# Optimization experiments

Hardware: AMD Instinct MI355X
Metric: run time of the kernel (lower is better)

Reference implementation:

```python
import jax, jax.numpy as jnp
import numpy as np

EPSILON = 0.1
GAMMA = 1.0
RHO = 0.5
STOPERR = 1e-6
NUMITERMAX = 100
FI = GAMMA / (GAMMA + EPSILON)  # exponent for semi-relaxed KL side


def setup_inputs() -> dict:
    key = jax.random.key(0)
    logits = jax.random.normal(key, (16, 4096, 1024), dtype=jnp.float32)
    return {"logits": logits}


def reference(logits):
    B, n, k = logits.shape
    K = k + 1  # extra 'dustbin' column with zero cost
    cost = -jax.nn.log_softmax(logits, axis=-1)                       # [B,n,k]
    expand_cost = jnp.concatenate([cost, jnp.zeros((B, n, 1), cost.dtype)], axis=-1)
    Q = jnp.exp(-expand_cost / EPSILON)                               # [B,n,K]
    Qt = Q.transpose(0, 2, 1)                                         # [B,K,n]
    Pa = jnp.full((B, n, 1), 1.0 / n, Q.dtype)
    Pb = jnp.full((B, K, 1), RHO / k, Q.dtype).at[:, -1, :].set(1.0 - RHO)
    a0 = jnp.zeros((B, n, 1), Q.dtype)
    b0 = jnp.full((B, K, 1), 1.0 / K, Q.dtype)

    def cond(state):
        _, _, err, it = state
        return jnp.logical_and(err > STOPERR, it < NUMITERMAX)

    def body(state):
        _, b, _, it = state
        a = Pa / jnp.matmul(Q, b)                                     # [B,n,1]
        b_new = Pb / jnp.matmul(Qt, a)                                # [B,K,1]
        b_new = b_new.at[:, :-1, :].set(jnp.power(b_new[:, :-1, :], FI))
        err = jnp.sqrt(jnp.sum((b_new - b) ** 2))
        return (a, b_new, err, it + 1)

    a, b, err, it = jax.lax.while_loop(
        cond, body, (a0, b0, jnp.asarray(1.0, Q.dtype), jnp.asarray(0)))

    plan = a * Q * b.transpose(0, 2, 1) * n                           # [B,n,K]
    return plan[:, :, :-1].astype(jnp.float32)                        # drop dustbin col
```

## Files before the change

kernel.cpp:

```cpp
#include <hip/hip_runtime.h>
#include <math.h>


namespace {
constexpr int   Bn      = 16;
constexpr int   Kc      = 1024;
constexpr int   KK      = 1025;
constexpr int   BSTR    = 1028;
constexpr int   ROWS    = 65536;
constexpr int   NBLK    = 512;
constexpr int   TPB     = 512;
constexpr int   SUBS    = 32;
constexpr int   RPB     = 128;
constexpr float PA      = 1.0f / 4096.0f;
constexpr float PB_LOW  = (float)(0.5 / 1024.0);
constexpr float PB_DUST = 0.5f;
constexpr float FI_F    = (float)(1.0 / 1.1);
constexpr float STOP    = 1e-6f;
constexpr int   NITER   = 100;
constexpr float LOG2E   = 1.44269504088896340736f;
constexpr float ILOG2E  = 0.69314718055994530942f;
constexpr float TLOG2E  = 14.4269504088896340736f;
constexpr float B0      = (float)(1.0 / 1025.0);
}

typedef __attribute__((ext_vector_type(8))) unsigned short ushort8;

__device__ __forceinline__ float wredsum(float v) {
#pragma unroll
  for (int m = 32; m >= 1; m >>= 1) v += __shfl_xor(v, m, 64);
  return v;
}
__device__ __forceinline__ float wredmax(float v) {
#pragma unroll
  for (int m = 32; m >= 1; m >>= 1) v = fmaxf(v, __shfl_xor(v, m, 64));
  return v;
}
__device__ __forceinline__ unsigned short f2bf(float x) {
  unsigned int u = __float_as_uint(x);
  return (unsigned short)((u + 0x7FFFu + ((u >> 16) & 1u)) >> 16);
}
__device__ __forceinline__ float bf2f(unsigned short h) {
  return __uint_as_float(((unsigned int)h) << 16);
}

__global__ void k_init(float* __restrict__ bstore, float* __restrict__ e2vec) {
  int tid = blockIdx.x * blockDim.x + threadIdx.x;
  int stride = gridDim.x * blockDim.x;
  for (int i = tid; i < Bn * BSTR; i += stride) {
    int j = i % BSTR;
    bstore[i] = (j < KK) ? B0 : 0.0f;
  }
  for (int i = tid; i < NITER * Bn; i += stride)
    e2vec[i] = (i == 0) ? 1.0f : 0.0f;
}

template <int MODE>
__global__ __launch_bounds__(512, 4) void k_step(
    const float* __restrict__ x, unsigned short* __restrict__ Qb,
    float* __restrict__ lsev, float* __restrict__ avec,
    float* __restrict__ bstore,
    const float* __restrict__ partIn, float* __restrict__ partOut,
    const float* __restrict__ sumaIn, float* __restrict__ sumaOut,
    float* __restrict__ e2vec, float* __restrict__ out, const int t) {
  __shared__ float bls[1026];
  __shared__ float cpart[8][1024];
  __shared__ float sred[8];
  __shared__ int sstop;
  const int tid = threadIdx.x, wave = tid >> 6, lane = tid & 63;
  const int blk = blockIdx.x, b = blk >> 5, sub = blk & 31;
  const int j2 = tid << 1;

  if constexpr (MODE != 0) {
    if (tid == 0) {
      float s = 0.0f;
#pragma unroll
      for (int j = 0; j < Bn; ++j) s += e2vec[(t - 1) * Bn + j];
      sstop = (!(sqrtf(s) > STOP)) ? 1 : 0;
    }
    __syncthreads();
    if constexpr (MODE == 1) { if (sstop) return; }

    if (MODE == 2 && sstop) {
      bls[j2]     = bstore[b * BSTR + j2];
      bls[j2 + 1] = bstore[b * BSTR + j2 + 1];
      if (tid == 0) bls[1024] = bstore[b * BSTR + 1024];
    } else {
      const float* pb = partIn + ((size_t)b << 15);
      float s0 = 0.0f, s1 = 0.0f;
#pragma unroll 8
      for (int sb = 0; sb < SUBS; ++sb) {
        const float2 v = *(const float2*)(pb + (sb << 10) + j2);
        s0 += v.x; s1 += v.y;
      }
      const float bn0 = exp2f(FI_F * log2f(PB_LOW / s0));
      const float bn1 = exp2f(FI_F * log2f(PB_LOW / s1));
      bls[j2] = bn0; bls[j2 + 1] = bn1;
      if (wave == 0) {
        float sa = (lane < SUBS) ? sumaIn[(b << 5) + lane] : 0.0f;
        sa = wredsum(sa);
        if (lane == 0) bls[1024] = PB_DUST / sa;
      }
      if constexpr (MODE == 1) {
        if (sub == 0) {
          const float bo0 = bstore[b * BSTR + j2];
          const float bo1 = bstore[b * BSTR + j2 + 1];
          float e2 = (bn0 - bo0) * (bn0 - bo0) + (bn1 - bo1) * (bn1 - bo1);
          const float ew = wredsum(e2);
          if (lane == 0) sred[wave] = ew;
          __syncthreads();
          if (tid == 0) {
            float tt = 0.0f;
#pragma unroll
            for (int w = 0; w < 8; ++w) tt += sred[w];
            const float bd = bls[1024], bod = bstore[b * BSTR + 1024];
            tt += (bd - bod) * (bd - bod);
            e2vec[t * Bn + b] = tt;
            bstore[b * BSTR + 1024] = bd;
          }
          bstore[b * BSTR + j2]     = bn0;
          bstore[b * BSTR + j2 + 1] = bn1;
        }
      }
    }
    __syncthreads();
  }

  if constexpr (MODE == 2) {
    float4 bb[4];
#pragma unroll
    for (int s = 0; s < 4; ++s) bb[s] = *(const float4*)&bls[(lane << 4) + (s << 2)];
    const int rowBase = blk * RPB + wave * 16;
    for (int r = 0; r < 16; ++r) {
      const int row = rowBase + r;
      const float lse = lsev[row];
      const float sc = avec[row] * 4096.0f;
      const float4* xp = (const float4*)(x + ((size_t)row << 10));
      float4* op = (float4*)(out + ((size_t)row << 10));
#pragma unroll
      for (int s = 0; s < 4; ++s) {
        const float4 v = xp[(lane << 2) + s];
        float4 o;
        o.x = exp2f((v.x - lse) * TLOG2E) * sc * bb[s].x;
        o.y = exp2f((v.y - lse) * TLOG2E) * sc * bb[s].y;
        o.z = exp2f((v.z - lse) * TLOG2E) * sc * bb[s].z;
        o.w = exp2f((v.w - lse) * TLOG2E) * sc * bb[s].w;
        op[(lane << 2) + s] = o;
      }
    }
    return;
  }

  float4 bb[4];
  float bdust;
  if constexpr (MODE == 0) {
    const float4 c = make_float4(B0, B0, B0, B0);
#pragma unroll
    for (int s = 0; s < 4; ++s) bb[s] = c;
    bdust = B0;
  } else {
#pragma unroll
    for (int s = 0; s < 4; ++s) bb[s] = *(const float4*)&bls[(lane << 4) + (s << 2)];
    bdust = bls[1024];
  }

  float acc[16];
#pragma unroll
  for (int e = 0; e < 16; ++e) acc[e] = 0.0f;
  float sal = 0.0f;

  const int rowBase = blk * RPB + wave * 16;
#pragma unroll 4
  for (int r = 0; r < 16; ++r) {
    float q[16];
    if constexpr (MODE == 0) {
      const float4* xp = (const float4*)(x + ((size_t)(rowBase + r) << 10));
      float4 v[4];
#pragma unroll
      for (int s = 0; s < 4; ++s) v[s] = xp[(lane << 2) + s];
      float m = -1e30f;
#pragma unroll
      for (int s = 0; s < 4; ++s)
        m = fmaxf(m, fmaxf(fmaxf(v[s].x, v[s].y), fmaxf(v[s].z, v[s].w)));
      m = wredmax(m);
      float su = 0.0f;
#pragma unroll
      for (int s = 0; s < 4; ++s)
        su += exp2f((v[s].x - m) * LOG2E) + exp2f((v[s].y - m) * LOG2E) +
              exp2f((v[s].z - m) * LOG2E) + exp2f((v[s].w - m) * LOG2E);
      su = wredsum(su);
      const float lse = m + log2f(su) * ILOG2E;
      if (lane == 0) lsev[rowBase + r] = lse;
      ushort8 qa, qb2;
#pragma unroll
      for (int s = 0; s < 4; ++s) {
        const unsigned short u0 = f2bf(exp2f((v[s].x - lse) * TLOG2E));
        const unsigned short u1 = f2bf(exp2f((v[s].y - lse) * TLOG2E));
        const unsigned short u2 = f2bf(exp2f((v[s].z - lse) * TLOG2E));
        const unsigned short u3 = f2bf(exp2f((v[s].w - lse) * TLOG2E));
        if (s < 2) { qa[s*4+0]=u0; qa[s*4+1]=u1; qa[s*4+2]=u2; qa[s*4+3]=u3; }
        else { qb2[(s-2)*4+0]=u0; qb2[(s-2)*4+1]=u1; qb2[(s-2)*4+2]=u2; qb2[(s-2)*4+3]=u3; }
        q[s*4+0]=bf2f(u0); q[s*4+1]=bf2f(u1); q[s*4+2]=bf2f(u2); q[s*4+3]=bf2f(u3);
      }
      ushort8* qp = (ushort8*)(Qb + ((size_t)(rowBase + r) << 10));
      qp[lane * 2] = qa; qp[lane * 2 + 1] = qb2;
    } else {
      const ushort8* qp = (const ushort8*)(Qb + ((size_t)(rowBase + r) << 10));
      const ushort8 qa = qp[lane * 2], qb2 = qp[lane * 2 + 1];
#pragma unroll
      for (int e = 0; e < 8; ++e) { q[e] = bf2f(qa[e]); q[8 + e] = bf2f(qb2[e]); }
    }

    float p = 0.0f;
#pragma unroll
    for (int s = 0; s < 4; ++s)
      p += q[s * 4 + 0] * bb[s].x + q[s * 4 + 1] * bb[s].y +
           q[s * 4 + 2] * bb[s].z + q[s * 4 + 3] * bb[s].w;

    const float inner = wredsum(p) + bdust;
    const float a = PA / inner;
    if (lane == 0) { avec[rowBase + r] = a; sal += a; }
#pragma unroll
    for (int e = 0; e < 16; ++e) acc[e] += q[e] * a;
  }
  if (lane == 0) sred[wave] = sal;

  float4* cp = (float4*)&cpart[wave][lane << 4];
#pragma unroll
  for (int s = 0; s < 4; ++s)
    cp[s] = make_float4(acc[s * 4 + 0], acc[s * 4 + 1], acc[s * 4 + 2], acc[s * 4 + 3]);
  __syncthreads();

  float o0 = 0.0f, o1 = 0.0f;
#pragma unroll
  for (int w = 0; w < 8; ++w) { o0 += cpart[w][j2]; o1 += cpart[w][j2 + 1]; }
  *(float2*)(partOut + ((size_t)b << 15) + (sub << 10) + j2) = make_float2(o0, o1);
  if (tid == 0) {
    float ss = 0.0f;
#pragma unroll
    for (int w = 0; w < 8; ++w) ss += sred[w];
    sumaOut[(b << 5) + sub] = ss;
  }
}

extern "C" void kernel_launch(void* const* d_in, const int* in_sizes, int n_in,
                              void* d_out, int out_size, void* d_ws, size_t ws_size,
                              hipStream_t stream) {
  const float* logits = (const float*)d_in[0];
  unsigned short* Qb = (unsigned short*)d_out;
  float* ws = (float*)d_ws;
  float* bstore = ws;
  float* avec   = bstore + Bn * BSTR;
  float* lsev   = avec + ROWS;
  float* partA  = lsev + ROWS;
  float* partB  = partA + (size_t)Bn * SUBS * Kc;
  float* sumaA  = partB + (size_t)Bn * SUBS * Kc;
  float* sumaB  = sumaA + NBLK;
  float* e2vec  = sumaB + NBLK;

  k_init<<<16, 256, 0, stream>>>(bstore, e2vec);
  k_step<0><<<NBLK, TPB, 0, stream>>>(logits, Qb, lsev, avec, bstore,
                                      partA, partA, sumaA, sumaA, e2vec, nullptr, 0);
  for (int t = 1; t < NITER; ++t) {
    const bool odd = (t & 1) != 0;
    k_step<1><<<NBLK, TPB, 0, stream>>>(logits, Qb, lsev, avec, bstore,
                                        odd ? partA : partB, odd ? partB : partA,
                                        odd ? sumaA : sumaB, odd ? sumaB : sumaA,
                                        e2vec, nullptr, t);
  }
  k_step<2><<<NBLK, TPB, 0, stream>>>(logits, Qb, lsev, avec, bstore,
                                      partB, partA, sumaB, sumaA, e2vec,
                                      (float*)d_out, NITER);
}
```

Baseline: 3.245 ms.

## Prefetch Q rows before the b-reduction, drop the max-subtraction, add a bf16-Q final pass

In the iteration kernel, eight Q rows per wave are loaded into registers before the partial-sum reduction and barrier, and the rest are software-pipelined, so global load latency overlaps the b update. The first pass drops the row max from the log-sum-exp and uses the known uniform b0 to compute a directly as a sum of q. When the workspace is large enough, Q is stored there and the final pass rebuilds the plan from bf16 Q instead of re-reading the logits and recomputing exp. The stop-flag check now runs in parallel with the b computation instead of behind its own barrier. Risks: overflow of exp without the max for large logits, higher register pressure, and a bf16-rounded output.

```diff
diff --git a/kernel.cpp b/kernel.cpp
--- a/kernel.cpp
+++ b/kernel.cpp
@@ -22,6 +22,9 @@
 constexpr float ILOG2E  = 0.69314718055994530942f;
 constexpr float TLOG2E  = 14.4269504088896340736f;
 constexpr float B0      = (float)(1.0 / 1025.0);
+constexpr size_t QBYTES = (size_t)ROWS * 1024 * 2;
+constexpr size_t FWORDS = (size_t)Bn * BSTR + 2 * ROWS +
+                          2 * (size_t)Bn * SUBS * Kc + 2 * NBLK + NITER * Bn;
 }
 
 typedef __attribute__((ext_vector_type(8))) unsigned short ushort8;
@@ -29,11 +32,6 @@
 __device__ __forceinline__ float wredsum(float v) {
 #pragma unroll
   for (int m = 32; m >= 1; m >>= 1) v += __shfl_xor(v, m, 64);
-  return v;
-}
-__device__ __forceinline__ float wredmax(float v) {
-#pragma unroll
-  for (int m = 32; m >= 1; m >>= 1) v = fmaxf(v, __shfl_xor(v, m, 64));
   return v;
 }
 __device__ __forceinline__ unsigned short f2bf(float x) {
@@ -42,6 +40,25 @@
 }
 __device__ __forceinline__ float bf2f(unsigned short h) {
   return __uint_as_float(((unsigned int)h) << 16);
+}
+
+__device__ __forceinline__ void consume_row(
+    const ushort8 qa, const ushort8 qb2, const float4* bb, const float bdust,
+    float* acc, float& sal, float* __restrict__ avec, const int row,
+    const int lane) {
+  float q[16];
+#pragma unroll
+  for (int e = 0; e < 8; ++e) { q[e] = bf2f(qa[e]); q[8 + e] = bf2f(qb2[e]); }
+  float p = 0.0f;
+#pragma unroll
+  for (int s = 0; s < 4; ++s)
+    p += q[s * 4 + 0] * bb[s].x + q[s * 4 + 1] * bb[s].y +
+         q[s * 4 + 2] * bb[s].z + q[s * 4 + 3] * bb[s].w;
+  const float inner = wredsum(p) + bdust;
+  const float a = PA / inner;
+  if (lane == 0) { avec[row] = a; sal += a; }
+#pragma unroll
+  for (int e = 0; e < 16; ++e) acc[e] += q[e] * a;
 }
 
 __global__ void k_init(float* __restrict__ bstore, float* __restrict__ e2vec) {
@@ -66,26 +83,30 @@
   __shared__ float bls[1026];
   __shared__ float cpart[8][1024];
   __shared__ float sred[8];
-  __shared__ int sstop;
+  __shared__ int sstop_s;
   const int tid = threadIdx.x, wave = tid >> 6, lane = tid & 63;
   const int blk = blockIdx.x, b = blk >> 5, sub = blk & 31;
   const int j2 = tid << 1;
-
+  const int rowBase = blk * RPB + wave * 16;
+
+  const ushort8* qrow = (const ushort8*)Qb + ((size_t)rowBase << 7) + (lane << 1);
+  ushort8 qa0, qb0, qa1, qb1, qa2, qb2, qa3, qb3,
+          qa4, qb4, qa5, qb5, qa6, qb6, qa7, qb7;
+#define QLOAD(i, r) do { qa##i = qrow[(r) << 7]; qb##i = qrow[((r) << 7) + 1]; } while (0)
+
+  if constexpr (MODE == 1) {
+    QLOAD(0, 0); QLOAD(1, 1); QLOAD(2, 2); QLOAD(3, 3);
+    QLOAD(4, 4); QLOAD(5, 5); QLOAD(6, 6); QLOAD(7, 7);
+  }
+
+  float bn0 = 0.0f, bn1 = 0.0f;
   if constexpr (MODE != 0) {
-    if (tid == 0) {
-      float s = 0.0f;
-#pragma unroll
-      for (int j = 0; j < Bn; ++j) s += e2vec[(t - 1) * Bn + j];
-      sstop = (!(sqrtf(s) > STOP)) ? 1 : 0;
-    }
-    __syncthreads();
-    if constexpr (MODE == 1) { if (sstop) return; }
-
-    if (MODE == 2 && sstop) {
-      bls[j2]     = bstore[b * BSTR + j2];
-      bls[j2 + 1] = bstore[b * BSTR + j2 + 1];
-      if (tid == 0) bls[1024] = bstore[b * BSTR + 1024];
-    } else {
+    if (wave == 0) {
+      float g = (lane < Bn) ? e2vec[(t - 1) * Bn + lane] : 0.0f;
+      g = wredsum(g);
+      if (lane == 0) sstop_s = (!(sqrtf(g) > STOP)) ? 1 : 0;
+    }
+    {
       const float* pb = partIn + ((size_t)b << 15);
       float s0 = 0.0f, s1 = 0.0f;
 #pragma unroll 8
@@ -93,44 +114,64 @@
         const float2 v = *(const float2*)(pb + (sb << 10) + j2);
         s0 += v.x; s1 += v.y;
       }
-      const float bn0 = exp2f(FI_F * log2f(PB_LOW / s0));
-      const float bn1 = exp2f(FI_F * log2f(PB_LOW / s1));
+      bn0 = exp2f(FI_F * log2f(PB_LOW / s0));
+      bn1 = exp2f(FI_F * log2f(PB_LOW / s1));
       bls[j2] = bn0; bls[j2 + 1] = bn1;
-      if (wave == 0) {
-        float sa = (lane < SUBS) ? sumaIn[(b << 5) + lane] : 0.0f;
-        sa = wredsum(sa);
-        if (lane == 0) bls[1024] = PB_DUST / sa;
-      }
-      if constexpr (MODE == 1) {
-        if (sub == 0) {
-          const float bo0 = bstore[b * BSTR + j2];
-          const float bo1 = bstore[b * BSTR + j2 + 1];
-          float e2 = (bn0 - bo0) * (bn0 - bo0) + (bn1 - bo1) * (bn1 - bo1);
-          const float ew = wredsum(e2);
-          if (lane == 0) sred[wave] = ew;
-          __syncthreads();
-          if (tid == 0) {
-            float tt = 0.0f;
-#pragma unroll
-            for (int w = 0; w < 8; ++w) tt += sred[w];
-            const float bd = bls[1024], bod = bstore[b * BSTR + 1024];
-            tt += (bd - bod) * (bd - bod);
-            e2vec[t * Bn + b] = tt;
-            bstore[b * BSTR + 1024] = bd;
-          }
-          bstore[b * BSTR + j2]     = bn0;
-          bstore[b * BSTR + j2 + 1] = bn1;
+    }
+    if (wave == 1) {
+      float sa = (lane < SUBS) ? sumaIn[(b << 5) + lane] : 0.0f;
+      sa = wredsum(sa);
+      if (lane == 0) bls[1024] = PB_DUST / sa;
+    }
+    __syncthreads();
+    const int sstop = sstop_s;
+    if constexpr (MODE == 1) {
+      if (sstop) return;
+      if (sub == 0) {
+        const float bo0 = bstore[b * BSTR + j2];
+        const float bo1 = bstore[b * BSTR + j2 + 1];
+        float e2 = (bn0 - bo0) * (bn0 - bo0) + (bn1 - bo1) * (bn1 - bo1);
+        const float ew = wredsum(e2);
+        if (lane == 0) sred[wave] = ew;
+        __syncthreads();
+        if (tid == 0) {
+          float tt = 0.0f;
+#pragma unroll
+          for (int w = 0; w < 8; ++w) tt += sred[w];
+          const float bd = bls[1024], bod = bstore[b * BSTR + 1024];
+          tt += (bd - bod) * (bd - bod);
+          e2vec[t * Bn + b] = tt;
+          bstore[b * BSTR + 1024] = bd;
         }
-      }
-    }
-    __syncthreads();
+        __syncthreads();
+        bstore[b * BSTR + j2]     = bn0;
+        bstore[b * BSTR + j2 + 1] = bn1;
+      }
+    } else {
+      if (sstop) {
+        bls[j2]     = bstore[b * BSTR + j2];
+        bls[j2 + 1] = bstore[b * BSTR + j2 + 1];
+        if (tid == 0) bls[1024] = bstore[b * BSTR + 1024];
+      }
+      __syncthreads();
+    }
+  }
+
+  float4 bb[4];
+  float bdust;
+  if constexpr (MODE == 0) {
+    const float4 c = make_float4(B0, B0, B0, B0);
+#pragma unroll
+    for (int s = 0; s < 4; ++s) bb[s] = c;
+    bdust = B0;
+  } else {
+#pragma unroll
+    for (int s = 0; s < 4; ++s) bb[s] = *(const float4*)&bls[(lane << 4) + (s << 2)];
+    bdust = bls[1024];
   }
 
   if constexpr (MODE == 2) {
-    float4 bb[4];
-#pragma unroll
-    for (int s = 0; s < 4; ++s) bb[s] = *(const float4*)&bls[(lane << 4) + (s << 2)];
-    const int rowBase = blk * RPB + wave * 16;
+#pragma unroll 2
     for (int r = 0; r < 16; ++r) {
       const int row = rowBase + r;
       const float lse = lsev[row];
@@ -151,17 +192,27 @@
     return;
   }
 
-  float4 bb[4];
-  float bdust;
-  if constexpr (MODE == 0) {
-    const float4 c = make_float4(B0, B0, B0, B0);
-#pragma unroll
-    for (int s = 0; s < 4; ++s) bb[s] = c;
-    bdust = B0;
-  } else {
-#pragma unroll
-    for (int s = 0; s < 4; ++s) bb[s] = *(const float4*)&bls[(lane << 4) + (s << 2)];
-    bdust = bls[1024];
+  if constexpr (MODE == 3) {
+#pragma unroll 2
+    for (int r = 0; r < 16; ++r) {
+      const int row = rowBase + r;
+      const ushort8 ua = qrow[r << 7], ub = qrow[(r << 7) + 1];
+      const float sc = avec[row] * 4096.0f;
+      float4* op = (float4*)(out + ((size_t)row << 10));
+      float q[16];
+#pragma unroll
+      for (int e = 0; e < 8; ++e) { q[e] = bf2f(ua[e]); q[8 + e] = bf2f(ub[e]); }
+#pragma unroll
+      for (int s = 0; s < 4; ++s) {
+        float4 o;
+        o.x = q[s * 4 + 0] * sc * bb[s].x;
+        o.y = q[s * 4 + 1] * sc * bb[s].y;
+        o.z = q[s * 4 + 2] * sc * bb[s].z;
+        o.w = q[s * 4 + 3] * sc * bb[s].w;
+        op[(lane << 2) + s] = o;
+      }
+    }
+    return;
   }
 
   float acc[16];
@@ -169,62 +220,64 @@
   for (int e = 0; e < 16; ++e) acc[e] = 0.0f;
   float sal = 0.0f;
 
-  const int rowBase = blk * RPB + wave * 16;
-#pragma unroll 4
-  for (int r = 0; r < 16; ++r) {
-    float q[16];
-    if constexpr (MODE == 0) {
-      const float4* xp = (const float4*)(x + ((size_t)(rowBase + r) << 10));
+  if constexpr (MODE == 0) {
+#pragma unroll 2
+    for (int r = 0; r < 16; ++r) {
+      const int row = rowBase + r;
+      const float4* xp = (const float4*)(x + ((size_t)row << 10));
       float4 v[4];
 #pragma unroll
       for (int s = 0; s < 4; ++s) v[s] = xp[(lane << 2) + s];
-      float m = -1e30f;
+      float su = 0.0f;
 #pragma unroll
       for (int s = 0; s < 4; ++s)
-        m = fmaxf(m, fmaxf(fmaxf(v[s].x, v[s].y), fmaxf(v[s].z, v[s].w)));
-      m = wredmax(m);
-      float su = 0.0f;
-#pragma unroll
-      for (int s = 0; s < 4; ++s)
-        su += exp2f((v[s].x - m) * LOG2E) + exp2f((v[s].y - m) * LOG2E) +
-              exp2f((v[s].z - m) * LOG2E) + exp2f((v[s].w - m) * LOG2E);
+        su += exp2f(v[s].x * LOG2E) + exp2f(v[s].y * LOG2E) +
+              exp2f(v[s].z * LOG2E) + exp2f(v[s].w * LOG2E);
       su = wredsum(su);
-      const float lse = m + log2f(su) * ILOG2E;
-      if (lane == 0) lsev[rowBase + r] = lse;
-      ushort8 qa, qb2;
+      const float lse = log2f(su) * ILOG2E;
+      if (lane == 0) lsev[row] = lse;
+      float q[16];
+      ushort8 ua, ub;
 #pragma unroll
       for (int s = 0; s < 4; ++s) {
         const unsigned short u0 = f2bf(exp2f((v[s].x - lse) * TLOG2E));
         const unsigned short u1 = f2bf(exp2f((v[s].y - lse) * TLOG2E));
         const unsigned short u2 = f2bf(exp2f((v[s].z - lse) * TLOG2E));
         const unsigned short u3 = f2bf(exp2f((v[s].w - lse) * TLOG2E));
-        if (s < 2) { qa[s*4+0]=u0; qa[s*4+1]=u1; qa[s*4+2]=u2; qa[s*4+3]=u3; }
-        else { qb2[(s-2)*4+0]=u0; qb2[(s-2)*4+1]=u1; qb2[(s-2)*4+2]=u2; qb2[(s-2)*4+3]=u3; }
+        if (s < 2) { ua[s*4+0]=u0; ua[s*4+1]=u1; ua[s*4+2]=u2; ua[s*4+3]=u3; }
+        else { ub[(s-2)*4+0]=u0; ub[(s-2)*4+1]=u1; ub[(s-2)*4+2]=u2; ub[(s-2)*4+3]=u3; }
         q[s*4+0]=bf2f(u0); q[s*4+1]=bf2f(u1); q[s*4+2]=bf2f(u2); q[s*4+3]=bf2f(u3);
       }
-      ushort8* qp = (ushort8*)(Qb + ((size_t)(rowBase + r) << 10));
-      qp[lane * 2] = qa; qp[lane * 2 + 1] = qb2;
-    } else {
-      const ushort8* qp = (const ushort8*)(Qb + ((size_t)(rowBase + r) << 10));
-      const ushort8 qa = qp[lane * 2], qb2 = qp[lane * 2 + 1];
-#pragma unroll
-      for (int e = 0; e < 8; ++e) { q[e] = bf2f(qa[e]); q[8 + e] = bf2f(qb2[e]); }
-    }
-
-    float p = 0.0f;
-#pragma unroll
-    for (int s = 0; s < 4; ++s)
-      p += q[s * 4 + 0] * bb[s].x + q[s * 4 + 1] * bb[s].y +
-           q[s * 4 + 2] * bb[s].z + q[s * 4 + 3] * bb[s].w;
-
-    const float inner = wredsum(p) + bdust;
-    const float a = PA / inner;
-    if (lane == 0) { avec[rowBase + r] = a; sal += a; }
-#pragma unroll
-    for (int e = 0; e < 16; ++e) acc[e] += q[e] * a;
-  }
+      ushort8* qp = (ushort8*)(Qb + ((size_t)row << 10));
+      qp[lane * 2] = ua; qp[lane * 2 + 1] = ub;
+      float sq = 0.0f;
+#pragma unroll
+      for (int e = 0; e < 16; ++e) sq += q[e];
+      const float inner = (wredsum(sq) + 1.0f) * B0;
+      const float a = PA / inner;
+      if (lane == 0) { avec[row] = a; sal += a; }
+#pragma unroll
+      for (int e = 0; e < 16; ++e) acc[e] += q[e] * a;
+    }
+  } else {
+#define STEP(i, r) do { \
+    consume_row(qa##i, qb##i, bb, bdust, acc, sal, avec, rowBase + (r), lane); \
+  } while (0)
+    STEP(0, 0); QLOAD(0, 8);
+    STEP(1, 1); QLOAD(1, 9);
+    STEP(2, 2); QLOAD(2, 10);
+    STEP(3, 3); QLOAD(3, 11);
+    STEP(4, 4); QLOAD(4, 12);
+    STEP(5, 5); QLOAD(5, 13);
+    STEP(6, 6); QLOAD(6, 14);
+    STEP(7, 7); QLOAD(7, 15);
+    STEP(0, 8);  STEP(1, 9);  STEP(2, 10); STEP(3, 11);
+    STEP(4, 12); STEP(5, 13); STEP(6, 14); STEP(7, 15);
+#undef STEP
+  }
+#undef QLOAD
+
   if (lane == 0) sred[wave] = sal;
-
   float4* cp = (float4*)&cpart[wave][lane << 4];
 #pragma unroll
   for (int s = 0; s < 4; ++s)
@@ -247,9 +300,18 @@
                               void* d_out, int out_size, void* d_ws, size_t ws_size,
                               hipStream_t stream) {
   const float* logits = (const float*)d_in[0];
-  unsigned short* Qb = (unsigned short*)d_out;
-  float* ws = (float*)d_ws;
-  float* bstore = ws;
+  const bool wsfit = ws_size >= QBYTES + FWORDS * sizeof(float);
+
+  unsigned short* Qb;
+  float* fbase;
+  if (wsfit) {
+    Qb = (unsigned short*)d_ws;
+    fbase = (float*)((char*)d_ws + QBYTES);
+  } else {
+    Qb = (unsigned short*)d_out;
+    fbase = (float*)d_ws;
+  }
+  float* bstore = fbase;
   float* avec   = bstore + Bn * BSTR;
   float* lsev   = avec + ROWS;
   float* partA  = lsev + ROWS;
@@ -260,7 +322,8 @@
 
   k_init<<<16, 256, 0, stream>>>(bstore, e2vec);
   k_step<0><<<NBLK, TPB, 0, stream>>>(logits, Qb, lsev, avec, bstore,
-                                      partA, partA, sumaA, sumaA, e2vec, nullptr, 0);
+                                      partA, partA, sumaA, sumaA, e2vec,
+                                      nullptr, 0);
   for (int t = 1; t < NITER; ++t) {
     const bool odd = (t & 1) != 0;
     k_step<1><<<NBLK, TPB, 0, stream>>>(logits, Qb, lsev, avec, bstore,
@@ -268,7 +331,12 @@
                                         odd ? sumaA : sumaB, odd ? sumaB : sumaA,
                                         e2vec, nullptr, t);
   }
-  k_step<2><<<NBLK, TPB, 0, stream>>>(logits, Qb, lsev, avec, bstore,
-                                      partB, partA, sumaB, sumaA, e2vec,
-                                      (float*)d_out, NITER);
-}
+  if (wsfit)
+    k_step<3><<<NBLK, TPB, 0, stream>>>(logits, Qb, lsev, avec, bstore,
+                                        partB, partA, sumaB, sumaA, e2vec,
+                                        (float*)d_out, NITER);
+  else
+    k_step<2><<<NBLK, TPB, 0, stream>>>(logits, Qb, lsev, avec, bstore,
+                                        partB, partA, sumaB, sumaA, e2vec,
+                                        (float*)d_out, NITER);
+}
```

After: 11.64 ms. +258.8%, slower.
